# Optimization experiments

Hardware: AMD Instinct MI355X
Metric: run time of the kernel (lower is better)

## Reference

```python
import jax, jax.numpy as jnp
import numpy as np

CLAMP_MIN = 1e-12
CLAMP_MAX = 1e12


def setup_inputs() -> dict:
    key = jax.random.key(0)
    k1, k2, k3 = jax.random.split(key, 3)
    N, D, C = 16384, 512, 10000
    features = jax.random.normal(k1, (N, D), dtype=jnp.float32)
    labels = jax.random.randint(k2, (N, 2), 0, C, dtype=jnp.int64)
    # torch.rand -> uniform [0,1)
    centers = jax.random.uniform(k3, (C, D), dtype=jnp.float32)
    return {"features": features, "labels": labels, "centers": centers}


def reference(features, labels, centers):
    # labels[:, -1] selects the class id per sample
    cls = labels[:, -1]
    # Original computes full cdist(features, centers)**2 then masks to the
    # label-matched entry per row. Mathematically that is ||f_i - c_{y_i}||^2,
    # so we gather the matching center and reduce directly (O(N*D)).
    c = centers[cls]                      # [N, D] gather
    diff = features - c                   # [N, D]
    d2 = jnp.sum(diff * diff, axis=-1)    # [N] squared L2 distance
    d2 = jnp.clip(d2, CLAMP_MIN, CLAMP_MAX)
    return jnp.mean(d2)
```

## Files before the change

### kernel.cpp

```cpp
#include <hip/hip_runtime.h>

#define N_ROWS 16384
#define DIM 512
#define NBLK 4096
#define ROWS_PER_WAVE 4

typedef float f32x4 __attribute__((ext_vector_type(4)));


__global__ __launch_bounds__(64) void centerloss_partial(
    const float* __restrict__ features,
    const int* __restrict__ labels,
    const float* __restrict__ centers,
    float* __restrict__ partials)
{
    const int lane = threadIdx.x;
    const int base = blockIdx.x * ROWS_PER_WAVE;

    int cls0 = labels[(base + 0) * 2 + 1];
    int cls1 = labels[(base + 1) * 2 + 1];
    int cls2 = labels[(base + 2) * 2 + 1];
    int cls3 = labels[(base + 3) * 2 + 1];

    const f32x4* __restrict__ f4 =
        reinterpret_cast<const f32x4*>(features + (size_t)base * DIM);
    f32x4 fa0 = __builtin_nontemporal_load(&f4[lane +   0]);
    f32x4 fb0 = __builtin_nontemporal_load(&f4[lane +  64]);
    f32x4 fa1 = __builtin_nontemporal_load(&f4[lane + 128]);
    f32x4 fb1 = __builtin_nontemporal_load(&f4[lane + 192]);
    f32x4 fa2 = __builtin_nontemporal_load(&f4[lane + 256]);
    f32x4 fb2 = __builtin_nontemporal_load(&f4[lane + 320]);
    f32x4 fa3 = __builtin_nontemporal_load(&f4[lane + 384]);
    f32x4 fb3 = __builtin_nontemporal_load(&f4[lane + 448]);

    const f32x4* __restrict__ c0 =
        reinterpret_cast<const f32x4*>(centers + (size_t)cls0 * DIM);
    const f32x4* __restrict__ c1 =
        reinterpret_cast<const f32x4*>(centers + (size_t)cls1 * DIM);
    const f32x4* __restrict__ c2 =
        reinterpret_cast<const f32x4*>(centers + (size_t)cls2 * DIM);
    const f32x4* __restrict__ c3 =
        reinterpret_cast<const f32x4*>(centers + (size_t)cls3 * DIM);
    f32x4 ca0 = c0[lane];  f32x4 cb0 = c0[lane + 64];
    f32x4 ca1 = c1[lane];  f32x4 cb1 = c1[lane + 64];
    f32x4 ca2 = c2[lane];  f32x4 cb2 = c2[lane + 64];
    f32x4 ca3 = c3[lane];  f32x4 cb3 = c3[lane + 64];

    f32x4 d;
    f32x4 vsum;
    d = fa0 - ca0; vsum  = d * d;
    d = fb0 - cb0; vsum += d * d;
    d = fa1 - ca1; vsum += d * d;
    d = fb1 - cb1; vsum += d * d;
    d = fa2 - ca2; vsum += d * d;
    d = fb2 - cb2; vsum += d * d;
    d = fa3 - ca3; vsum += d * d;
    d = fb3 - cb3; vsum += d * d;

    float lsum = vsum.x + vsum.y + vsum.z + vsum.w;

    #pragma unroll
    for (int off = 1; off < 64; off <<= 1)
        lsum += __shfl_xor(lsum, off, 64);

    if (lane == 0) partials[blockIdx.x] = lsum;
}

__global__ __launch_bounds__(256) void centerloss_final(
    const float* __restrict__ partials, float* __restrict__ out)
{
    const float4* __restrict__ p4 = reinterpret_cast<const float4*>(partials);
    float s = 0.f;
    #pragma unroll
    for (int k = 0; k < NBLK / 4 / 256; ++k) {
        float4 v = p4[threadIdx.x + k * 256];
        s += v.x + v.y + v.z + v.w;
    }

    #pragma unroll
    for (int off = 1; off < 64; off <<= 1)
        s += __shfl_xor(s, off, 64);

    __shared__ float smem[4];
    const int lane = threadIdx.x & 63;
    const int wave = threadIdx.x >> 6;
    if (lane == 0) smem[wave] = s;
    __syncthreads();
    if (threadIdx.x == 0) {
        float t = smem[0] + smem[1] + smem[2] + smem[3];
        out[0] = t / (float)N_ROWS;
    }
}

extern "C" void kernel_launch(void* const* d_in, const int* in_sizes, int n_in,
                              void* d_out, int out_size, void* d_ws, size_t ws_size,
                              hipStream_t stream)
{
    const float* features = (const float*)d_in[0];
    const int*   labels   = (const int*)d_in[1];
    const float* centers  = (const float*)d_in[2];
    float* out = (float*)d_out;
    float* partials = (float*)d_ws;

    centerloss_partial<<<NBLK, 64, 0, stream>>>(features, labels, centers, partials);
    centerloss_final<<<1, 256, 0, stream>>>(partials, out);
}
```

Measured before the change: 16.38 us.

## Fuse partial and final reduction into one kernel with magic-tagged slots

Merges the two-kernel reduction into one launch. Each 512-thread block reduces its 8 waves in shared memory and publishes its partial to a global slot tagged with a magic word. Block 0 then spins until all 512 slots are tagged, sums them and resets the slots for the next call. This removes the second kernel launch and its dependency gap, at the cost of a spin-wait that assumes every block is eventually scheduled and of larger blocks with fewer waves in flight.

```diff
diff --git a/kernel.cpp b/kernel.cpp
--- a/kernel.cpp
+++ b/kernel.cpp
@@ -2,20 +2,26 @@
 
 #define N_ROWS 16384
 #define DIM 512
-#define NBLK 4096
+#define NBLK 512
+#define NTHR 512
+#define WAVES_PER_BLK (NTHR / 64)
 #define ROWS_PER_WAVE 4
+#define MAGIC 0x5AC0FFEEu
 
 typedef float f32x4 __attribute__((ext_vector_type(4)));
 
 
-__global__ __launch_bounds__(64) void centerloss_partial(
+__global__ __launch_bounds__(NTHR) void centerloss_onepass(
     const float* __restrict__ features,
     const int* __restrict__ labels,
     const float* __restrict__ centers,
-    float* __restrict__ partials)
+    float* __restrict__ out,
+    unsigned long long* __restrict__ slots)
 {
-    const int lane = threadIdx.x;
-    const int base = blockIdx.x * ROWS_PER_WAVE;
+    const int lane  = threadIdx.x & 63;
+    const int wid   = threadIdx.x >> 6;
+    const int gwave = blockIdx.x * WAVES_PER_BLK + wid;
+    const int base  = gwave * ROWS_PER_WAVE;
 
     int cls0 = labels[(base + 0) * 2 + 1];
     int cls1 = labels[(base + 1) * 2 + 1];
@@ -46,8 +52,7 @@
     f32x4 ca2 = c2[lane];  f32x4 cb2 = c2[lane + 64];
     f32x4 ca3 = c3[lane];  f32x4 cb3 = c3[lane + 64];
 
-    f32x4 d;
-    f32x4 vsum;
+    f32x4 d, vsum;
     d = fa0 - ca0; vsum  = d * d;
     d = fb0 - cb0; vsum += d * d;
     d = fa1 - ca1; vsum += d * d;
@@ -63,31 +68,44 @@
     for (int off = 1; off < 64; off <<= 1)
         lsum += __shfl_xor(lsum, off, 64);
 
-    if (lane == 0) partials[blockIdx.x] = lsum;
-}
+    __shared__ float smem[WAVES_PER_BLK];
+    if (lane == 0) smem[wid] = lsum;
+    __syncthreads();
 
-__global__ __launch_bounds__(256) void centerloss_final(
-    const float* __restrict__ partials, float* __restrict__ out)
-{
-    const float4* __restrict__ p4 = reinterpret_cast<const float4*>(partials);
-    float s = 0.f;
-    #pragma unroll
-    for (int k = 0; k < NBLK / 4 / 256; ++k) {
-        float4 v = p4[threadIdx.x + k * 256];
-        s += v.x + v.y + v.z + v.w;
+    if (threadIdx.x == 0) {
+        float b = 0.f;
+        #pragma unroll
+        for (int w = 0; w < WAVES_PER_BLK; ++w) b += smem[w];
+        unsigned long long v =
+            ((unsigned long long)__float_as_uint(b) << 32) | (unsigned long long)MAGIC;
+        __hip_atomic_store(&slots[blockIdx.x], v,
+                           __ATOMIC_RELAXED, __HIP_MEMORY_SCOPE_AGENT);
     }
+
+    if (blockIdx.x != 0) return;
+
+    unsigned long long v;
+    for (;;) {
+        v = __hip_atomic_load(&slots[threadIdx.x],
+                              __ATOMIC_RELAXED, __HIP_MEMORY_SCOPE_AGENT);
+        if ((unsigned)v == MAGIC) break;
+        __builtin_amdgcn_s_sleep(2);
+    }
+    float p = __uint_as_float((unsigned)(v >> 32));
+    __hip_atomic_store(&slots[threadIdx.x], 0ull,
+                       __ATOMIC_RELAXED, __HIP_MEMORY_SCOPE_AGENT);
 
     #pragma unroll
     for (int off = 1; off < 64; off <<= 1)
-        s += __shfl_xor(s, off, 64);
+        p += __shfl_xor(p, off, 64);
 
-    __shared__ float smem[4];
-    const int lane = threadIdx.x & 63;
-    const int wave = threadIdx.x >> 6;
-    if (lane == 0) smem[wave] = s;
+    __shared__ float smem2[WAVES_PER_BLK];
+    if (lane == 0) smem2[wid] = p;
     __syncthreads();
     if (threadIdx.x == 0) {
-        float t = smem[0] + smem[1] + smem[2] + smem[3];
+        float t = 0.f;
+        #pragma unroll
+        for (int w = 0; w < WAVES_PER_BLK; ++w) t += smem2[w];
         out[0] = t / (float)N_ROWS;
     }
 }
@@ -100,8 +118,7 @@
     const int*   labels   = (const int*)d_in[1];
     const float* centers  = (const float*)d_in[2];
     float* out = (float*)d_out;
-    float* partials = (float*)d_ws;
+    unsigned long long* slots = (unsigned long long*)d_ws;
 
-    centerloss_partial<<<NBLK, 64, 0, stream>>>(features, labels, centers, partials);
-    centerloss_final<<<1, 256, 0, stream>>>(partials, out);
+    centerloss_onepass<<<NBLK, NTHR, 0, stream>>>(features, labels, centers, out, slots);
 }
```

Measured after the change: 15.17 us (median of 2 runs). 1.08x faster.
